# Kernel tuning notes

Measured on AMD Instinct MI355X. Metric: run time of the kernel, lower is better.

## Reference

```python
import jax, jax.numpy as jnp
import numpy as np

N = 50000      # nodes
E = 500000     # edges
IN_FEAT = 128
OUT_FEAT = 128
R = 200        # num_relations
NB = 16        # num_bases -> 8x8 blocks
SI = IN_FEAT // NB   # submat_in = 8
SO = OUT_FEAT // NB  # submat_out = 8


def setup_inputs() -> dict:
    key = jax.random.key(0)
    k1, k2, k3, k4, k5, k6, k7 = jax.random.split(key, 7)
    h = jax.random.normal(k1, (N, IN_FEAT), dtype=jnp.float32)
    norm = jax.random.uniform(k2, (N, 1), dtype=jnp.float32)
    weight = jax.random.normal(k3, (R, NB * SI * SO), dtype=jnp.float32) * 0.1
    loop_weight = jax.random.normal(k4, (IN_FEAT, OUT_FEAT), dtype=jnp.float32) * 0.1
    src = jax.random.randint(k5, (E,), 0, N, dtype=jnp.int32)
    dst = jax.random.randint(k6, (E,), 0, N, dtype=jnp.int32)
    etype = jax.random.randint(k7, (E,), 0, R, dtype=jnp.int32)
    return {"h": h, "norm": norm, "weight": weight, "loop_weight": loop_weight,
            "src": src, "dst": dst, "etype": etype}


def reference(h, norm, weight, loop_weight, src, dst, etype):
    # self-loop message: [N, out_feat]
    loop_message = h @ loop_weight
    # per-edge relation-weight gather: [E, NB, SI, SO]
    w_e = weight[etype].reshape(-1, NB, SI, SO)
    # src features as per-basis blocks: [E, NB, SI]
    x_e = h[src].reshape(-1, NB, SI)
    # block-diagonal bmm -> messages [E, out_feat]
    msg = jnp.einsum('ebi,ebio->ebo', x_e, w_e).reshape(-1, OUT_FEAT)
    # scatter-sum to destination nodes (fn.sum(msg -> h))
    agg = jax.ops.segment_sum(msg, dst, num_segments=N)
    # apply_func: multiply by per-node norm, then add self-loop and activation
    nodes = agg * norm
    nodes = nodes + loop_message
    return jax.nn.relu(nodes)
```

## Files before the change

### kernel.cpp

```cpp
#include <hip/hip_runtime.h>
#include <hip/hip_bf16.h>


#define IN_FEAT 128
#define OUT_FEAT 128
#define SCAN_CHUNK 512

using short8  = __attribute__((ext_vector_type(8))) short;
using float4v = __attribute__((ext_vector_type(4))) float;

__device__ inline float blo(unsigned u) { return __uint_as_float(u << 16); }
__device__ inline float bhi(unsigned u) { return __uint_as_float(u & 0xffff0000u); }
__device__ inline unsigned short f2bf(float f) {
  __hip_bfloat16 b = __float2bfloat16(f);
  return *reinterpret_cast<unsigned short*>(&b);
}

__device__ inline float dot2bf(unsigned x, unsigned w, float c) {
#if __has_builtin(__builtin_amdgcn_fdot2_f32_bf16)
  typedef __bf16 bf16x2 __attribute__((ext_vector_type(2)));
  return __builtin_amdgcn_fdot2_f32_bf16(__builtin_bit_cast(bf16x2, x),
                                         __builtin_bit_cast(bf16x2, w), c, false);
#else
  return c + blo(x) * blo(w) + bhi(x) * bhi(w);
#endif
}

__global__ __launch_bounds__(256) void k_prep(
    const float* __restrict__ w, unsigned short* __restrict__ w16,
    const float* __restrict__ h, uint4* __restrict__ h16p, int htotal8,
    const float* __restrict__ lw, unsigned short* __restrict__ lwT,
    const int* __restrict__ dst, int* __restrict__ cnt, int E,
    int bw, int bh, int blw) {
  __shared__ float srow[1024];
  const int bid = blockIdx.x;
  if (bid < bw) {
    const float* wr = w + ((size_t)bid << 10);
    ((float4*)srow)[threadIdx.x] = ((const float4*)wr)[threadIdx.x];
    __syncthreads();
    const int d0 = threadIdx.x * 4;
    unsigned short o4[4];
    #pragma unroll
    for (int k = 0; k < 4; ++k) {
      const int d = d0 + k;
      const int b = d >> 6;
      const int q = d & 63;
      const int opp = q >> 4;
      const int tt = q & 15;
      const int jj = tt >> 3;
      const int ii = tt & 7;
      o4[k] = f2bf(srow[b * 64 + ii * 8 + opp * 2 + jj]);
    }
    *(uint2*)(w16 + ((size_t)bid << 10) + d0) =
        make_uint2((unsigned)o4[0] | ((unsigned)o4[1] << 16),
                   (unsigned)o4[2] | ((unsigned)o4[3] << 16));
  } else if (bid < bw + bh) {
    const int t = (bid - bw) * 256 + threadIdx.x;
    if (t < htotal8) {
      const float4 a = ((const float4*)h)[2 * t];
      const float4 b = ((const float4*)h)[2 * t + 1];
      uint4 o;
      o.x = (unsigned)f2bf(a.x) | ((unsigned)f2bf(a.y) << 16);
      o.y = (unsigned)f2bf(a.z) | ((unsigned)f2bf(a.w) << 16);
      o.z = (unsigned)f2bf(b.x) | ((unsigned)f2bf(b.y) << 16);
      o.w = (unsigned)f2bf(b.z) | ((unsigned)f2bf(b.w) << 16);
      h16p[t] = o;
    }
  } else if (bid < bw + bh + blw) {
    const int idx = (bid - bw - bh) * 256 + threadIdx.x;
    if (idx < IN_FEAT * OUT_FEAT) {
      const int o = idx >> 7;
      const int k = idx & 127;
      lwT[idx] = f2bf(lw[k * 128 + o]);
    }
  } else {
    const int e0 = ((bid - bw - bh - blw) * 256 + threadIdx.x) * 4;
    if (e0 + 3 < E) {
      const int4 d4 = *(const int4*)(dst + e0);
      atomicAdd(&cnt[d4.x], 1);
      atomicAdd(&cnt[d4.y], 1);
      atomicAdd(&cnt[d4.z], 1);
      atomicAdd(&cnt[d4.w], 1);
    } else {
      for (int e = e0; e < E; ++e) atomicAdd(&cnt[dst[e]], 1);
    }
  }
}

__global__ __launch_bounds__(256) void k_gemm_sum(
    const unsigned short* __restrict__ h16, const unsigned short* __restrict__ lwT,
    float* __restrict__ out, int N,
    const int* __restrict__ cnt, int* __restrict__ bsum, int gemm_blocks) {
  if (blockIdx.x < gemm_blocks) {
    const int wid = threadIdx.x >> 6;
    const int lane = threadIdx.x & 63;
    const int row0 = blockIdx.x * 64 + wid * 16;
    if (row0 >= N) return;
    const int m = lane & 15;
    const int kg = (lane >> 4) * 8;
    const int arow = min(row0 + m, N - 1);

    float4v acc[8];
    #pragma unroll
    for (int nt = 0; nt < 8; ++nt) acc[nt] = (float4v){0.f, 0.f, 0.f, 0.f};

    const unsigned short* ap = h16 + (size_t)arow * 128 + kg;
    const unsigned short* bp = lwT + (size_t)m * 128 + kg;

    #pragma unroll
    for (int kc = 0; kc < 4; ++kc) {
      const short8 a = *(const short8*)(ap + kc * 32);
      #pragma unroll
      for (int nt = 0; nt < 8; ++nt) {
        const short8 b = *(const short8*)(bp + nt * 2048 + kc * 32);
        acc[nt] = __builtin_amdgcn_mfma_f32_16x16x32_bf16(a, b, acc[nt], 0, 0, 0);
      }
    }

    const int crow = row0 + (lane >> 4) * 4;
    #pragma unroll
    for (int nt = 0; nt < 8; ++nt) {
      #pragma unroll
      for (int r = 0; r < 4; ++r) {
        const int row = crow + r;
        if (row < N) out[(size_t)row * 128 + nt * 16 + m] = acc[nt][r];
      }
    }
  } else {
    __shared__ int s[256];
    const int cb = blockIdx.x - gemm_blocks;
    const int t = threadIdx.x;
    const int base = cb * SCAN_CHUNK;
    int v = 0;
    const int i0 = base + t, i1 = base + 256 + t;
    if (i0 < N) v += cnt[i0];
    if (i1 < N) v += cnt[i1];
    s[t] = v;
    __syncthreads();
    for (int d = 128; d > 0; d >>= 1) {
      if (t < d) s[t] += s[t + d];
      __syncthreads();
    }
    if (t == 0) bsum[cb] = s[0];
  }
}

__global__ __launch_bounds__(256) void k_chunksum(
    const int* __restrict__ cnt, int* __restrict__ bsum, int N) {
  __shared__ int s[256];
  const int t = threadIdx.x;
  const int base = blockIdx.x * SCAN_CHUNK;
  int v = 0;
  int i0 = base + t, i1 = base + 256 + t;
  if (i0 < N) v += cnt[i0];
  if (i1 < N) v += cnt[i1];
  s[t] = v;
  __syncthreads();
  for (int d = 128; d > 0; d >>= 1) {
    if (t < d) s[t] += s[t + d];
    __syncthreads();
  }
  if (t == 0) bsum[blockIdx.x] = s[0];
}

__global__ __launch_bounds__(256) void k_hist(
    const int* __restrict__ dst, int* __restrict__ cnt, int E) {
  const int e = blockIdx.x * blockDim.x + threadIdx.x;
  if (e < E) atomicAdd(&cnt[dst[e]], 1);
}

__global__ __launch_bounds__(256) void k_offsets(
    const int* __restrict__ cnt, const int* __restrict__ bsum,
    int* __restrict__ pos, int N) {
  __shared__ int s[256];
  __shared__ int sbase;
  const int t = threadIdx.x;
  if (t < 64) {
    int acc = 0;
    for (int j = t; j < (int)blockIdx.x; j += 64) acc += bsum[j];
    #pragma unroll
    for (int d = 1; d < 64; d <<= 1) acc += __shfl_xor(acc, d);
    if (t == 0) sbase = acc;
  }
  const int base = blockIdx.x * SCAN_CHUNK;
  const int i0 = base + 2 * t;
  const int i1 = i0 + 1;
  const int c0 = (i0 < N) ? cnt[i0] : 0;
  const int c1 = (i1 < N) ? cnt[i1] : 0;
  const int pair = c0 + c1;
  s[t] = pair;
  __syncthreads();
  #pragma unroll
  for (int d = 1; d < 256; d <<= 1) {
    int v = (t >= d) ? s[t - d] : 0;
    __syncthreads();
    s[t] += v;
    __syncthreads();
  }
  const int ex = s[t] - pair + sbase;
  if (i0 < N) pos[i0] = ex;
  if (i1 < N) pos[i1] = ex + c0;
}

__global__ __launch_bounds__(256) void k_scatter(
    const int* __restrict__ src, const int* __restrict__ dst,
    const int* __restrict__ etype, int* __restrict__ pos,
    int2* __restrict__ srcet, int E) {
  const int e0 = (blockIdx.x * blockDim.x + threadIdx.x) * 4;
  if (e0 + 3 < E) {
    const int4 s4 = *(const int4*)(src + e0);
    const int4 d4 = *(const int4*)(dst + e0);
    const int4 t4 = *(const int4*)(etype + e0);
    int p;
    p = atomicAdd(&pos[d4.x], 1); srcet[p] = make_int2(s4.x, t4.x);
    p = atomicAdd(&pos[d4.y], 1); srcet[p] = make_int2(s4.y, t4.y);
    p = atomicAdd(&pos[d4.z], 1); srcet[p] = make_int2(s4.z, t4.z);
    p = atomicAdd(&pos[d4.w], 1); srcet[p] = make_int2(s4.w, t4.w);
  } else {
    for (int e = e0; e < E; ++e) {
      const int p = atomicAdd(&pos[dst[e]], 1);
      srcet[p] = make_int2(src[e], etype[e]);
    }
  }
}

__global__ __launch_bounds__(256) void agg_bf16(
    const unsigned short* __restrict__ h16, const float* __restrict__ norm,
    const unsigned short* __restrict__ w16, const int* __restrict__ pos,
    const int* __restrict__ cnt, const int2* __restrict__ srcet,
    float* __restrict__ out, int N) {
  const int node = (int)((blockIdx.x * blockDim.x + threadIdx.x) >> 6);
  const int lane = threadIdx.x & 63;
  if (node >= N) return;

  const int b = lane >> 2;
  const int opp = lane & 3;
  const int woff = b * 64 + opp * 16;
  const int o = b * 8 + opp * 2;

  const int num = cnt[node];
  const int end = pos[node];
  const int begin = end - num;

  float* outp = out + ((size_t)node << 7) + o;
  const float2 prev = *(const float2*)outp;
  const float nm = norm[node];

  float a0 = 0.f, a1 = 0.f;

  for (int base = 0; base < num; base += 64) {
    const int cn = min(64, num - base);
    const int2 my = srcet[begin + base + min(lane, cn - 1)];
    for (int i4 = 0; i4 < cn; i4 += 4) {
      const int gl = min(i4 + (lane >> 4), cn - 1);
      const int sg = __shfl(my.x, gl);
      const uint4 xq =
          *(const uint4*)(h16 + ((size_t)sg << 7) + (lane & 15) * 8);
      const int nin = min(4, cn - i4);
      #pragma unroll 4
      for (int u = 0; u < nin; ++u) {
        const int r = __shfl(my.y, i4 + u);
        const int sl = u * 16 + b;
        uint4 xv;
        xv.x = __shfl(xq.x, sl);
        xv.y = __shfl(xq.y, sl);
        xv.z = __shfl(xq.z, sl);
        xv.w = __shfl(xq.w, sl);
        const unsigned short* wp = w16 + ((size_t)r << 10) + woff;
        const uint4 wa = *(const uint4*)(wp);
        const uint4 wb = *(const uint4*)(wp + 8);

        a0 = dot2bf(xv.x, wa.x, a0);
        a0 = dot2bf(xv.y, wa.y, a0);
        a0 = dot2bf(xv.z, wa.z, a0);
        a0 = dot2bf(xv.w, wa.w, a0);
        a1 = dot2bf(xv.x, wb.x, a1);
        a1 = dot2bf(xv.y, wb.y, a1);
        a1 = dot2bf(xv.z, wb.z, a1);
        a1 = dot2bf(xv.w, wb.w, a1);
      }
    }
  }

  float2 res;
  res.x = fmaxf(prev.x + a0 * nm, 0.f);
  res.y = fmaxf(prev.y + a1 * nm, 0.f);
  *(float2*)outp = res;
}

__global__ __launch_bounds__(256) void selfloop_gemm(
    const float* __restrict__ h, const float* __restrict__ lw,
    float* __restrict__ out, int n) {
  __shared__ float slw[IN_FEAT * OUT_FEAT];
  __shared__ float sh[32 * IN_FEAT];

  {
    const float4* s4 = (const float4*)lw;
    float4* d4 = (float4*)slw;
    for (int i = threadIdx.x; i < IN_FEAT * OUT_FEAT / 4; i += 256) d4[i] = s4[i];
  }

  const int cg = threadIdx.x & 31;
  const int rg = threadIdx.x >> 5;

  for (int base = blockIdx.x * 32; base < n; base += gridDim.x * 32) {
    const int nrows = min(32, n - base);
    __syncthreads();
    {
      const float4* hs = (const float4*)(h + (size_t)base * IN_FEAT);
      float4* sd = (float4*)sh;
      const int cnt = nrows * (IN_FEAT / 4);
      for (int i = threadIdx.x; i < cnt; i += 256) sd[i] = hs[i];
    }
    __syncthreads();

    float4 acc[4];
    #pragma unroll
    for (int j = 0; j < 4; ++j) acc[j] = make_float4(0.f, 0.f, 0.f, 0.f);

    #pragma unroll 4
    for (int k = 0; k < IN_FEAT; ++k) {
      const float4 w = ((const float4*)slw)[k * 32 + cg];
      #pragma unroll
      for (int j = 0; j < 4; ++j) {
        const float hv = sh[(rg + 8 * j) * IN_FEAT + k];
        acc[j].x += hv * w.x;
        acc[j].y += hv * w.y;
        acc[j].z += hv * w.z;
        acc[j].w += hv * w.w;
      }
    }

    #pragma unroll
    for (int j = 0; j < 4; ++j) {
      const int r = rg + 8 * j;
      if (r < nrows) {
        ((float4*)(out + (size_t)(base + r) * OUT_FEAT))[cg] = acc[j];
      }
    }
  }
}

__global__ __launch_bounds__(256) void agg(
    const float* __restrict__ h, const float* __restrict__ norm,
    const float* __restrict__ weight, const int* __restrict__ pos,
    const int* __restrict__ cnt, const int2* __restrict__ srcet,
    float* __restrict__ out, int N) {
  const int node = (int)((blockIdx.x * blockDim.x + threadIdx.x) >> 6);
  const int lane = threadIdx.x & 63;
  if (node >= N) return;

  const int b = lane >> 2;
  const int op = (lane & 3) * 2;
  const int boff = b * 64 + op;

  const int num = cnt[node];
  const int end = pos[node];
  const int begin = end - num;

  float a0 = 0.f, a1 = 0.f;

  for (int base = 0; base < num; base += 64) {
    const int cn = min(64, num - base);
    const int2 my = srcet[begin + base + min(lane, cn - 1)];
    #pragma unroll 2
    for (int i = 0; i < cn; ++i) {
      const int s = __shfl(my.x, i);
      const int r = __shfl(my.y, i);
      const float* xp = h + ((size_t)s << 7) + b * 8;
      const float4 x0 = ((const float4*)xp)[0];
      const float4 x1 = ((const float4*)xp)[1];
      const float* wp = weight + ((size_t)r << 10) + boff;
      const float2 w0 = *(const float2*)(wp);
      const float2 w1 = *(const float2*)(wp + 8);
      const float2 w2 = *(const float2*)(wp + 16);
      const float2 w3 = *(const float2*)(wp + 24);
      const float2 w4 = *(const float2*)(wp + 32);
      const float2 w5 = *(const float2*)(wp + 40);
      const float2 w6 = *(const float2*)(wp + 48);
      const float2 w7 = *(const float2*)(wp + 56);
      a0 += x0.x * w0.x; a1 += x0.x * w0.y;
      a0 += x0.y * w1.x; a1 += x0.y * w1.y;
      a0 += x0.z * w2.x; a1 += x0.z * w2.y;
      a0 += x0.w * w3.x; a1 += x0.w * w3.y;
      a0 += x1.x * w4.x; a1 += x1.x * w4.y;
      a0 += x1.y * w5.x; a1 += x1.y * w5.y;
      a0 += x1.z * w6.x; a1 += x1.z * w6.y;
      a0 += x1.w * w7.x; a1 += x1.w * w7.y;
    }
  }

  const float nm = norm[node];
  const int o = b * 8 + op;
  float* outp = out + ((size_t)node << 7) + o;
  float2 prev = *(const float2*)outp;
  float2 res;
  res.x = fmaxf(prev.x + a0 * nm, 0.f);
  res.y = fmaxf(prev.y + a1 * nm, 0.f);
  *(float2*)outp = res;
}

__global__ __launch_bounds__(256) void edge_msg(
    const float* __restrict__ h, const float* __restrict__ norm,
    const float* __restrict__ weight, const int* __restrict__ src,
    const int* __restrict__ dst, const int* __restrict__ etype,
    float* out, int E) {
  const int wave = (int)((blockIdx.x * blockDim.x + threadIdx.x) >> 6);
  const int lane = threadIdx.x & 63;
  if (wave >= E) return;

  const int s = src[wave];
  const int d = dst[wave];
  const int r = etype[wave];
  const float nrm = norm[d];

  const int b = lane >> 2;
  const int op = (lane & 3) * 2;

  const float* xp = h + (size_t)s * IN_FEAT + b * 8;
  const float4 x0 = ((const float4*)xp)[0];
  const float4 x1 = ((const float4*)xp)[1];
  float x[8] = {x0.x, x0.y, x0.z, x0.w, x1.x, x1.y, x1.z, x1.w};

  const float* wp = weight + (size_t)r * 1024 + b * 64 + op;
  float a0 = 0.f, a1 = 0.f;
  #pragma unroll
  for (int i = 0; i < 8; ++i) {
    const float2 w = *(const float2*)(wp + i * 8);
    a0 += x[i] * w.x;
    a1 += x[i] * w.y;
  }

  const int o = b * 8 + op;
  float* outp = out + (size_t)d * OUT_FEAT + o;
  atomicAdd(outp, a0 * nrm);
  atomicAdd(outp + 1, a1 * nrm);
}

__global__ __launch_bounds__(256) void relu_k(float* __restrict__ out, int n4) {
  const int i = blockIdx.x * blockDim.x + threadIdx.x;
  if (i < n4) {
    float4 v = ((const float4*)out)[i];
    v.x = fmaxf(v.x, 0.f);
    v.y = fmaxf(v.y, 0.f);
    v.z = fmaxf(v.z, 0.f);
    v.w = fmaxf(v.w, 0.f);
    ((float4*)out)[i] = v;
  }
}

extern "C" void kernel_launch(void* const* d_in, const int* in_sizes, int n_in,
                              void* d_out, int out_size, void* d_ws, size_t ws_size,
                              hipStream_t stream) {
  const float* h    = (const float*)d_in[0];
  const float* norm = (const float*)d_in[1];
  const float* w    = (const float*)d_in[2];
  const float* lw   = (const float*)d_in[3];
  const int* src    = (const int*)d_in[4];
  const int* dst    = (const int*)d_in[5];
  const int* etype  = (const int*)d_in[6];
  float* out = (float*)d_out;

  const int N = in_sizes[1];
  const int E = in_sizes[4];
  const int R = in_sizes[2] / 1024;
  const int nblk = (N + SCAN_CHUNK - 1) / SCAN_CHUNK;

  const size_t nb_bsum = (size_t)((nblk < 128) ? 128 : nblk);
  const size_t off_cnt  = (size_t)E * 8;
  const size_t off_pos  = off_cnt + (size_t)N * 4;
  const size_t off_bsum = off_pos + (size_t)N * 4;
  size_t off_h16 = off_bsum + nb_bsum * 4;
  off_h16 = (off_h16 + 15) & ~(size_t)15;
  const size_t off_w16 = off_h16 + (size_t)N * IN_FEAT * 2;
  const size_t off_lwT = off_w16 + (size_t)R * 1024 * 2;
  const size_t need_full = off_lwT + (size_t)IN_FEAT * OUT_FEAT * 2;
  const size_t need_sort = off_bsum + nb_bsum * 4;

  if (ws_size >= need_full) {
    char* wsb = (char*)d_ws;
    int2* srcet = (int2*)wsb;
    int* cnt  = (int*)(wsb + off_cnt);
    int* pos  = (int*)(wsb + off_pos);
    int* bsum = (int*)(wsb + off_bsum);
    unsigned short* h16 = (unsigned short*)(wsb + off_h16);
    unsigned short* w16 = (unsigned short*)(wsb + off_w16);
    unsigned short* lwT = (unsigned short*)(wsb + off_lwT);

    hipMemsetAsync(cnt, 0, (size_t)N * 4, stream);

    const int htotal8 = N * IN_FEAT / 8;
    const int bw  = R;
    const int bh  = (htotal8 + 255) / 256;
    const int blw = (IN_FEAT * OUT_FEAT + 255) / 256;
    const int bhist = (E + 1023) / 1024;
    k_prep<<<bw + bh + blw + bhist, 256, 0, stream>>>(
        w, w16, h, (uint4*)h16, htotal8, lw, lwT, dst, cnt, E, bw, bh, blw);

    const int gemm_blocks = (N + 63) / 64;
    k_gemm_sum<<<gemm_blocks + nblk, 256, 0, stream>>>(
        h16, lwT, out, N, cnt, bsum, gemm_blocks);

    k_offsets<<<nblk, 256, 0, stream>>>(cnt, bsum, pos, N);
    k_scatter<<<(E + 1023) / 1024, 256, 0, stream>>>(src, dst, etype, pos,
                                                     srcet, E);

    agg_bf16<<<(N + 3) / 4, 256, 0, stream>>>(h16, norm, w16, pos, cnt, srcet,
                                              out, N);
  } else if (ws_size >= need_sort) {
    char* wsb = (char*)d_ws;
    int2* srcet = (int2*)wsb;
    int* cnt  = (int*)(wsb + off_cnt);
    int* pos  = (int*)(wsb + off_pos);
    int* bsum = (int*)(wsb + off_bsum);

    selfloop_gemm<<<512, 256, 0, stream>>>(h, lw, out, N);
    hipMemsetAsync(cnt, 0, (size_t)N * 4, stream);
    k_hist<<<(E + 255) / 256, 256, 0, stream>>>(dst, cnt, E);
    k_chunksum<<<nblk, 256, 0, stream>>>(cnt, bsum, N);
    k_offsets<<<nblk, 256, 0, stream>>>(cnt, bsum, pos, N);
    k_scatter<<<(E + 1023) / 1024, 256, 0, stream>>>(src, dst, etype, pos,
                                                     srcet, E);
    agg<<<(N + 3) / 4, 256, 0, stream>>>(h, norm, w, pos, cnt, srcet, out, N);
  } else {
    selfloop_gemm<<<512, 256, 0, stream>>>(h, lw, out, N);
    edge_msg<<<(E + 3) / 4, 256, 0, stream>>>(h, norm, w, src, dst, etype, out, E);
    const int n4 = N * OUT_FEAT / 4;
    relu_k<<<(n4 + 255) / 256, 256, 0, stream>>>(out, n4);
  }
}
```

Measured before the change: 148.4 us.

## Fuse preprocessing, GEMM, histogram, scan and scatter into one cooperative kernel

Replaces the memset and the four preprocessing launches (bf16 conversion, self-loop MFMA GEMM plus count, offsets, scatter) with a single cooperative persistent kernel that separates phases with grid-wide syncs. The aim is to remove launch gaps and inter-kernel drain overhead. The scan now has each block re-sum all counts before its chunk instead of using a separate chunk-sum pass, which adds redundant reads. The grid is capped at occupancy, so each phase uses grid-stride loops, and the weight conversion is now done element by element. A fallback path keeps the old multi-kernel sequence when cooperative launch is unavailable.

```diff
diff --git a/kernel.cpp b/kernel.cpp
--- a/kernel.cpp
+++ b/kernel.cpp
@@ -1,5 +1,8 @@
 #include <hip/hip_runtime.h>
 #include <hip/hip_bf16.h>
+#include <hip/hip_cooperative_groups.h>
+
+namespace cg = cooperative_groups;
 
 
 #define IN_FEAT 128
@@ -24,6 +27,238 @@
 #else
   return c + blo(x) * blo(w) + bhi(x) * bhi(w);
 #endif
+}
+
+__global__ __launch_bounds__(256, 4) void k_pipeline(
+    const float* __restrict__ w, const float* __restrict__ h,
+    const float* __restrict__ lw, const int* __restrict__ src,
+    const int* __restrict__ dst, const int* __restrict__ etype,
+    unsigned short* __restrict__ w16, uint4* __restrict__ h16p,
+    unsigned short* __restrict__ lwT, int* __restrict__ cnt,
+    int* __restrict__ pos, int2* __restrict__ srcet,
+    float* __restrict__ out, int N, int E, int R) {
+  cg::grid_group grid = cg::this_grid();
+  const int nb = (int)gridDim.x;
+  const int tid = (int)threadIdx.x;
+  const int gtid = (int)blockIdx.x * 256 + tid;
+  const int gstride = nb * 256;
+
+  for (int i = gtid; i < N; i += gstride) cnt[i] = 0;
+
+  const int wtotal = R * 1024;
+  for (int idx = gtid; idx < wtotal; idx += gstride) {
+    const int r = idx >> 10;
+    const int rem = idx & 1023;
+    const int b = rem >> 6;
+    const int q = rem & 63;
+    const int opp = q >> 4;
+    const int t = q & 15;
+    const int j = t >> 3;
+    const int i = t & 7;
+    w16[idx] = f2bf(w[((size_t)r << 10) + b * 64 + i * 8 + opp * 2 + j]);
+  }
+
+  const int htotal8 = N * (IN_FEAT / 8);
+  for (int t8 = gtid; t8 < htotal8; t8 += gstride) {
+    const float4 a = ((const float4*)h)[2 * t8];
+    const float4 b = ((const float4*)h)[2 * t8 + 1];
+    uint4 o;
+    o.x = (unsigned)f2bf(a.x) | ((unsigned)f2bf(a.y) << 16);
+    o.y = (unsigned)f2bf(a.z) | ((unsigned)f2bf(a.w) << 16);
+    o.z = (unsigned)f2bf(b.x) | ((unsigned)f2bf(b.y) << 16);
+    o.w = (unsigned)f2bf(b.z) | ((unsigned)f2bf(b.w) << 16);
+    h16p[t8] = o;
+  }
+
+  for (int idx = gtid; idx < IN_FEAT * OUT_FEAT; idx += gstride) {
+    const int o = idx >> 7;
+    const int k = idx & 127;
+    lwT[idx] = f2bf(lw[k * 128 + o]);
+  }
+
+  grid.sync();
+
+  {
+    const unsigned short* h16 = (const unsigned short*)h16p;
+    const int wid = tid >> 6;
+    const int lane = tid & 63;
+    const int m = lane & 15;
+    const int kg = (lane >> 4) * 8;
+    const int gemm_vb = (N + 63) >> 6;
+    for (int vb = (int)blockIdx.x; vb < gemm_vb; vb += nb) {
+      const int row0 = vb * 64 + wid * 16;
+      if (row0 < N) {
+        const int arow = min(row0 + m, N - 1);
+        float4v acc[8];
+        #pragma unroll
+        for (int nt = 0; nt < 8; ++nt) acc[nt] = (float4v){0.f, 0.f, 0.f, 0.f};
+        const unsigned short* ap = h16 + (size_t)arow * 128 + kg;
+        const unsigned short* bp = lwT + (size_t)m * 128 + kg;
+        #pragma unroll
+        for (int kc = 0; kc < 4; ++kc) {
+          const short8 a = *(const short8*)(ap + kc * 32);
+          #pragma unroll
+          for (int nt = 0; nt < 8; ++nt) {
+            const short8 b = *(const short8*)(bp + nt * 2048 + kc * 32);
+            acc[nt] =
+                __builtin_amdgcn_mfma_f32_16x16x32_bf16(a, b, acc[nt], 0, 0, 0);
+          }
+        }
+        const int crow = row0 + (lane >> 4) * 4;
+        #pragma unroll
+        for (int nt = 0; nt < 8; ++nt) {
+          #pragma unroll
+          for (int r = 0; r < 4; ++r) {
+            const int row = crow + r;
+            if (row < N) out[(size_t)row * 128 + nt * 16 + m] = acc[nt][r];
+          }
+        }
+      }
+    }
+  }
+  {
+    const int e4 = (E + 3) >> 2;
+    for (int g = gtid; g < e4; g += gstride) {
+      const int e0 = g * 4;
+      if (e0 + 3 < E) {
+        const int4 d4 = *(const int4*)(dst + e0);
+        atomicAdd(&cnt[d4.x], 1);
+        atomicAdd(&cnt[d4.y], 1);
+        atomicAdd(&cnt[d4.z], 1);
+        atomicAdd(&cnt[d4.w], 1);
+      } else {
+        for (int e = e0; e < E; ++e) atomicAdd(&cnt[dst[e]], 1);
+      }
+    }
+  }
+
+  grid.sync();
+
+  {
+    __shared__ int s[256];
+    __shared__ int sbase;
+    const int nblk = (N + SCAN_CHUNK - 1) / SCAN_CHUNK;
+    for (int vb = (int)blockIdx.x; vb < nblk; vb += nb) {
+      __syncthreads();
+      const int lim = vb * SCAN_CHUNK;
+      int acc = 0;
+      for (int i = tid; i < lim; i += 256) acc += cnt[i];
+      s[tid] = acc;
+      __syncthreads();
+      for (int d = 128; d > 0; d >>= 1) {
+        if (tid < d) s[tid] += s[tid + d];
+        __syncthreads();
+      }
+      if (tid == 0) sbase = s[0];
+      __syncthreads();
+      const int base = vb * SCAN_CHUNK;
+      const int i0 = base + 2 * tid;
+      const int i1 = i0 + 1;
+      const int c0 = (i0 < N) ? cnt[i0] : 0;
+      const int c1 = (i1 < N) ? cnt[i1] : 0;
+      const int pair = c0 + c1;
+      s[tid] = pair;
+      __syncthreads();
+      #pragma unroll
+      for (int d = 1; d < 256; d <<= 1) {
+        int v = (tid >= d) ? s[tid - d] : 0;
+        __syncthreads();
+        s[tid] += v;
+        __syncthreads();
+      }
+      const int ex = s[tid] - pair + sbase;
+      if (i0 < N) pos[i0] = ex;
+      if (i1 < N) pos[i1] = ex + c0;
+    }
+  }
+
+  grid.sync();
+
+  {
+    const int e4 = (E + 3) >> 2;
+    for (int g = gtid; g < e4; g += gstride) {
+      const int e0 = g * 4;
+      if (e0 + 3 < E) {
+        const int4 s4 = *(const int4*)(src + e0);
+        const int4 d4 = *(const int4*)(dst + e0);
+        const int4 t4 = *(const int4*)(etype + e0);
+        int p;
+        p = atomicAdd(&pos[d4.x], 1); srcet[p] = make_int2(s4.x, t4.x);
+        p = atomicAdd(&pos[d4.y], 1); srcet[p] = make_int2(s4.y, t4.y);
+        p = atomicAdd(&pos[d4.z], 1); srcet[p] = make_int2(s4.z, t4.z);
+        p = atomicAdd(&pos[d4.w], 1); srcet[p] = make_int2(s4.w, t4.w);
+      } else {
+        for (int e = e0; e < E; ++e) {
+          const int p = atomicAdd(&pos[dst[e]], 1);
+          srcet[p] = make_int2(src[e], etype[e]);
+        }
+      }
+    }
+  }
+}
+
+__global__ __launch_bounds__(256) void agg_bf16(
+    const unsigned short* __restrict__ h16, const float* __restrict__ norm,
+    const unsigned short* __restrict__ w16, const int* __restrict__ pos,
+    const int* __restrict__ cnt, const int2* __restrict__ srcet,
+    float* __restrict__ out, int N) {
+  const int node = (int)((blockIdx.x * blockDim.x + threadIdx.x) >> 6);
+  const int lane = threadIdx.x & 63;
+  if (node >= N) return;
+
+  const int b = lane >> 2;
+  const int opp = lane & 3;
+  const int woff = b * 64 + opp * 16;
+  const int o = b * 8 + opp * 2;
+
+  const int num = cnt[node];
+  const int end = pos[node];
+  const int begin = end - num;
+
+  float* outp = out + ((size_t)node << 7) + o;
+  const float2 prev = *(const float2*)outp;
+  const float nm = norm[node];
+
+  float a0 = 0.f, a1 = 0.f;
+
+  for (int base = 0; base < num; base += 64) {
+    const int cn = min(64, num - base);
+    const int2 my = srcet[begin + base + min(lane, cn - 1)];
+    for (int i4 = 0; i4 < cn; i4 += 4) {
+      const int gl = min(i4 + (lane >> 4), cn - 1);
+      const int sg = __shfl(my.x, gl);
+      const uint4 xq =
+          *(const uint4*)(h16 + ((size_t)sg << 7) + (lane & 15) * 8);
+      const int nin = min(4, cn - i4);
+      #pragma unroll 4
+      for (int u = 0; u < nin; ++u) {
+        const int r = __shfl(my.y, i4 + u);
+        const int sl = u * 16 + b;
+        uint4 xv;
+        xv.x = __shfl(xq.x, sl);
+        xv.y = __shfl(xq.y, sl);
+        xv.z = __shfl(xq.z, sl);
+        xv.w = __shfl(xq.w, sl);
+        const unsigned short* wp = w16 + ((size_t)r << 10) + woff;
+        const uint4 wa = *(const uint4*)(wp);
+        const uint4 wb = *(const uint4*)(wp + 8);
+
+        a0 = dot2bf(xv.x, wa.x, a0);
+        a0 = dot2bf(xv.y, wa.y, a0);
+        a0 = dot2bf(xv.z, wa.z, a0);
+        a0 = dot2bf(xv.w, wa.w, a0);
+        a1 = dot2bf(xv.x, wb.x, a1);
+        a1 = dot2bf(xv.y, wb.y, a1);
+        a1 = dot2bf(xv.z, wb.z, a1);
+        a1 = dot2bf(xv.w, wb.w, a1);
+      }
+    }
+  }
+
+  float2 res;
+  res.x = fmaxf(prev.x + a0 * nm, 0.f);
+  res.y = fmaxf(prev.y + a1 * nm, 0.f);
+  *(float2*)outp = res;
 }
 
 __global__ __launch_bounds__(256) void k_prep(
@@ -145,30 +380,6 @@
   }
 }
 
-__global__ __launch_bounds__(256) void k_chunksum(
-    const int* __restrict__ cnt, int* __restrict__ bsum, int N) {
-  __shared__ int s[256];
-  const int t = threadIdx.x;
-  const int base = blockIdx.x * SCAN_CHUNK;
-  int v = 0;
-  int i0 = base + t, i1 = base + 256 + t;
-  if (i0 < N) v += cnt[i0];
-  if (i1 < N) v += cnt[i1];
-  s[t] = v;
-  __syncthreads();
-  for (int d = 128; d > 0; d >>= 1) {
-    if (t < d) s[t] += s[t + d];
-    __syncthreads();
-  }
-  if (t == 0) bsum[blockIdx.x] = s[0];
-}
-
-__global__ __launch_bounds__(256) void k_hist(
-    const int* __restrict__ dst, int* __restrict__ cnt, int E) {
-  const int e = blockIdx.x * blockDim.x + threadIdx.x;
-  if (e < E) atomicAdd(&cnt[dst[e]], 1);
-}
-
 __global__ __launch_bounds__(256) void k_offsets(
     const int* __restrict__ cnt, const int* __restrict__ bsum,
     int* __restrict__ pos, int N) {
@@ -224,68 +435,28 @@
   }
 }
 
-__global__ __launch_bounds__(256) void agg_bf16(
-    const unsigned short* __restrict__ h16, const float* __restrict__ norm,
-    const unsigned short* __restrict__ w16, const int* __restrict__ pos,
-    const int* __restrict__ cnt, const int2* __restrict__ srcet,
-    float* __restrict__ out, int N) {
-  const int node = (int)((blockIdx.x * blockDim.x + threadIdx.x) >> 6);
-  const int lane = threadIdx.x & 63;
-  if (node >= N) return;
-
-  const int b = lane >> 2;
-  const int opp = lane & 3;
-  const int woff = b * 64 + opp * 16;
-  const int o = b * 8 + opp * 2;
-
-  const int num = cnt[node];
-  const int end = pos[node];
-  const int begin = end - num;
-
-  float* outp = out + ((size_t)node << 7) + o;
-  const float2 prev = *(const float2*)outp;
-  const float nm = norm[node];
-
-  float a0 = 0.f, a1 = 0.f;
-
-  for (int base = 0; base < num; base += 64) {
-    const int cn = min(64, num - base);
-    const int2 my = srcet[begin + base + min(lane, cn - 1)];
-    for (int i4 = 0; i4 < cn; i4 += 4) {
-      const int gl = min(i4 + (lane >> 4), cn - 1);
-      const int sg = __shfl(my.x, gl);
-      const uint4 xq =
-          *(const uint4*)(h16 + ((size_t)sg << 7) + (lane & 15) * 8);
-      const int nin = min(4, cn - i4);
-      #pragma unroll 4
-      for (int u = 0; u < nin; ++u) {
-        const int r = __shfl(my.y, i4 + u);
-        const int sl = u * 16 + b;
-        uint4 xv;
-        xv.x = __shfl(xq.x, sl);
-        xv.y = __shfl(xq.y, sl);
-        xv.z = __shfl(xq.z, sl);
-        xv.w = __shfl(xq.w, sl);
-        const unsigned short* wp = w16 + ((size_t)r << 10) + woff;
-        const uint4 wa = *(const uint4*)(wp);
-        const uint4 wb = *(const uint4*)(wp + 8);
-
-        a0 = dot2bf(xv.x, wa.x, a0);
-        a0 = dot2bf(xv.y, wa.y, a0);
-        a0 = dot2bf(xv.z, wa.z, a0);
-        a0 = dot2bf(xv.w, wa.w, a0);
-        a1 = dot2bf(xv.x, wb.x, a1);
-        a1 = dot2bf(xv.y, wb.y, a1);
-        a1 = dot2bf(xv.z, wb.z, a1);
-        a1 = dot2bf(xv.w, wb.w, a1);
-      }
-    }
-  }
-
-  float2 res;
-  res.x = fmaxf(prev.x + a0 * nm, 0.f);
-  res.y = fmaxf(prev.y + a1 * nm, 0.f);
-  *(float2*)outp = res;
+__global__ __launch_bounds__(256) void k_hist(
+    const int* __restrict__ dst, int* __restrict__ cnt, int E) {
+  const int e = blockIdx.x * blockDim.x + threadIdx.x;
+  if (e < E) atomicAdd(&cnt[dst[e]], 1);
+}
+
+__global__ __launch_bounds__(256) void k_chunksum(
+    const int* __restrict__ cnt, int* __restrict__ bsum, int N) {
+  __shared__ int s[256];
+  const int t = threadIdx.x;
+  const int base = blockIdx.x * SCAN_CHUNK;
+  int v = 0;
+  int i0 = base + t, i1 = base + 256 + t;
+  if (i0 < N) v += cnt[i0];
+  if (i1 < N) v += cnt[i1];
+  s[t] = v;
+  __syncthreads();
+  for (int d = 128; d > 0; d >>= 1) {
+    if (t < d) s[t] += s[t + d];
+    __syncthreads();
+  }
+  if (t == 0) bsum[blockIdx.x] = s[0];
 }
 
 __global__ __launch_bounds__(256) void selfloop_gemm(
@@ -300,7 +471,7 @@
     for (int i = threadIdx.x; i < IN_FEAT * OUT_FEAT / 4; i += 256) d4[i] = s4[i];
   }
 
-  const int cg = threadIdx.x & 31;
+  const int cg_ = threadIdx.x & 31;
   const int rg = threadIdx.x >> 5;
 
   for (int base = blockIdx.x * 32; base < n; base += gridDim.x * 32) {
@@ -320,7 +491,7 @@
 
     #pragma unroll 4
     for (int k = 0; k < IN_FEAT; ++k) {
-      const float4 w = ((const float4*)slw)[k * 32 + cg];
+      const float4 w = ((const float4*)slw)[k * 32 + cg_];
       #pragma unroll
       for (int j = 0; j < 4; ++j) {
         const float hv = sh[(rg + 8 * j) * IN_FEAT + k];
@@ -335,7 +506,7 @@
     for (int j = 0; j < 4; ++j) {
       const int r = rg + 8 * j;
       if (r < nrows) {
-        ((float4*)(out + (size_t)(base + r) * OUT_FEAT))[cg] = acc[j];
+        ((float4*)(out + (size_t)(base + r) * OUT_FEAT))[cg_] = acc[j];
       }
     }
   }
@@ -487,26 +658,45 @@
     unsigned short* w16 = (unsigned short*)(wsb + off_w16);
     unsigned short* lwT = (unsigned short*)(wsb + off_lwT);
 
-    hipMemsetAsync(cnt, 0, (size_t)N * 4, stream);
-
-    const int htotal8 = N * IN_FEAT / 8;
-    const int bw  = R;
-    const int bh  = (htotal8 + 255) / 256;
-    const int blw = (IN_FEAT * OUT_FEAT + 255) / 256;
-    const int bhist = (E + 1023) / 1024;
-    k_prep<<<bw + bh + blw + bhist, 256, 0, stream>>>(
-        w, w16, h, (uint4*)h16, htotal8, lw, lwT, dst, cnt, E, bw, bh, blw);
-
-    const int gemm_blocks = (N + 63) / 64;
-    k_gemm_sum<<<gemm_blocks + nblk, 256, 0, stream>>>(
-        h16, lwT, out, N, cnt, bsum, gemm_blocks);
-
-    k_offsets<<<nblk, 256, 0, stream>>>(cnt, bsum, pos, N);
-    k_scatter<<<(E + 1023) / 1024, 256, 0, stream>>>(src, dst, etype, pos,
-                                                     srcet, E);
-
-    agg_bf16<<<(N + 3) / 4, 256, 0, stream>>>(h16, norm, w16, pos, cnt, srcet,
-                                              out, N);
+    int dev = 0;
+    hipGetDevice(&dev);
+    int coop = 0;
+    hipDeviceGetAttribute(&coop, hipDeviceAttributeCooperativeLaunch, dev);
+    int ncu = 0, maxb = 0;
+    if (coop) {
+      hipDeviceGetAttribute(&ncu, hipDeviceAttributeMultiprocessorCount, dev);
+      hipOccupancyMaxActiveBlocksPerMultiprocessor(&maxb, k_pipeline, 256, 0);
+    }
+    const int grid = ncu * maxb;
+
+    if (coop && grid > 0) {
+      uint4* h16p = (uint4*)h16;
+      void* args[] = {(void*)&w,   (void*)&h,    (void*)&lw,  (void*)&src,
+                      (void*)&dst, (void*)&etype,(void*)&w16, (void*)&h16p,
+                      (void*)&lwT, (void*)&cnt,  (void*)&pos, (void*)&srcet,
+                      (void*)&out, (void*)&N,    (void*)&E,   (void*)&R};
+      hipLaunchCooperativeKernel((void*)k_pipeline, dim3(grid), dim3(256),
+                                 args, 0, stream);
+      agg_bf16<<<(N + 3) / 4, 256, 0, stream>>>(h16, norm, w16, pos, cnt,
+                                                srcet, out, N);
+    } else {
+      hipMemsetAsync(cnt, 0, (size_t)N * 4, stream);
+      const int htotal8 = N * IN_FEAT / 8;
+      const int bw  = R;
+      const int bh  = (htotal8 + 255) / 256;
+      const int blw = (IN_FEAT * OUT_FEAT + 255) / 256;
+      const int bhist = (E + 1023) / 1024;
+      k_prep<<<bw + bh + blw + bhist, 256, 0, stream>>>(
+          w, w16, h, (uint4*)h16, htotal8, lw, lwT, dst, cnt, E, bw, bh, blw);
+      const int gemm_blocks = (N + 63) / 64;
+      k_gemm_sum<<<gemm_blocks + nblk, 256, 0, stream>>>(
+          h16, lwT, out, N, cnt, bsum, gemm_blocks);
+      k_offsets<<<nblk, 256, 0, stream>>>(cnt, bsum, pos, N);
+      k_scatter<<<(E + 1023) / 1024, 256, 0, stream>>>(src, dst, etype, pos,
+                                                       srcet, E);
+      agg_bf16<<<(N + 3) / 4, 256, 0, stream>>>(h16, norm, w16, pos, cnt,
+                                                srcet, out, N);
+    }
   } else if (ws_size >= need_sort) {
     char* wsb = (char*)d_ws;
     int2* srcet = (int2*)wsb;
```

New measurement: 328.6 us. +121.5%, slower.

## Fuse self-loop GEMM into aggregation kernel and drop separate chunk-sum pass

Applied to the files above, without the earlier changes.

Moves the self-loop h@loop_weight MFMA GEMM into the aggregation kernel. Each 256-thread block computes a 16-row tile into shared memory and then aggregates those 16 nodes, so the loop message is never written to and re-read from global memory. It also replaces the chunk-sum plus offsets pair with one offsets kernel, where each block recomputes its prefix by reading all earlier counts. That saves a launch and the global round trip, but the prefix work grows quadratically with block count, and each wave now handles 4 nodes serially, which may reduce latency hiding in the gather loop.

```diff
diff --git a/kernel.cpp b/kernel.cpp
--- a/kernel.cpp
+++ b/kernel.cpp
@@ -87,102 +87,26 @@
   }
 }
 
-__global__ __launch_bounds__(256) void k_gemm_sum(
-    const unsigned short* __restrict__ h16, const unsigned short* __restrict__ lwT,
-    float* __restrict__ out, int N,
-    const int* __restrict__ cnt, int* __restrict__ bsum, int gemm_blocks) {
-  if (blockIdx.x < gemm_blocks) {
-    const int wid = threadIdx.x >> 6;
-    const int lane = threadIdx.x & 63;
-    const int row0 = blockIdx.x * 64 + wid * 16;
-    if (row0 >= N) return;
-    const int m = lane & 15;
-    const int kg = (lane >> 4) * 8;
-    const int arow = min(row0 + m, N - 1);
-
-    float4v acc[8];
-    #pragma unroll
-    for (int nt = 0; nt < 8; ++nt) acc[nt] = (float4v){0.f, 0.f, 0.f, 0.f};
-
-    const unsigned short* ap = h16 + (size_t)arow * 128 + kg;
-    const unsigned short* bp = lwT + (size_t)m * 128 + kg;
-
-    #pragma unroll
-    for (int kc = 0; kc < 4; ++kc) {
-      const short8 a = *(const short8*)(ap + kc * 32);
-      #pragma unroll
-      for (int nt = 0; nt < 8; ++nt) {
-        const short8 b = *(const short8*)(bp + nt * 2048 + kc * 32);
-        acc[nt] = __builtin_amdgcn_mfma_f32_16x16x32_bf16(a, b, acc[nt], 0, 0, 0);
-      }
-    }
-
-    const int crow = row0 + (lane >> 4) * 4;
-    #pragma unroll
-    for (int nt = 0; nt < 8; ++nt) {
-      #pragma unroll
-      for (int r = 0; r < 4; ++r) {
-        const int row = crow + r;
-        if (row < N) out[(size_t)row * 128 + nt * 16 + m] = acc[nt][r];
-      }
-    }
-  } else {
-    __shared__ int s[256];
-    const int cb = blockIdx.x - gemm_blocks;
-    const int t = threadIdx.x;
-    const int base = cb * SCAN_CHUNK;
-    int v = 0;
-    const int i0 = base + t, i1 = base + 256 + t;
-    if (i0 < N) v += cnt[i0];
-    if (i1 < N) v += cnt[i1];
-    s[t] = v;
+__global__ __launch_bounds__(256) void k_offsets_sp(
+    const int* __restrict__ cnt, int* __restrict__ pos, int N) {
+  __shared__ int s[256];
+  __shared__ int sbase;
+  const int t = threadIdx.x;
+  const int vb = blockIdx.x;
+  {
+    const int lim = vb * SCAN_CHUNK;
+    int acc = 0;
+    for (int i = t; i < lim; i += 256) acc += cnt[i];
+    s[t] = acc;
     __syncthreads();
     for (int d = 128; d > 0; d >>= 1) {
       if (t < d) s[t] += s[t + d];
       __syncthreads();
     }
-    if (t == 0) bsum[cb] = s[0];
-  }
-}
-
-__global__ __launch_bounds__(256) void k_chunksum(
-    const int* __restrict__ cnt, int* __restrict__ bsum, int N) {
-  __shared__ int s[256];
-  const int t = threadIdx.x;
-  const int base = blockIdx.x * SCAN_CHUNK;
-  int v = 0;
-  int i0 = base + t, i1 = base + 256 + t;
-  if (i0 < N) v += cnt[i0];
-  if (i1 < N) v += cnt[i1];
-  s[t] = v;
-  __syncthreads();
-  for (int d = 128; d > 0; d >>= 1) {
-    if (t < d) s[t] += s[t + d];
-    __syncthreads();
-  }
-  if (t == 0) bsum[blockIdx.x] = s[0];
-}
-
-__global__ __launch_bounds__(256) void k_hist(
-    const int* __restrict__ dst, int* __restrict__ cnt, int E) {
-  const int e = blockIdx.x * blockDim.x + threadIdx.x;
-  if (e < E) atomicAdd(&cnt[dst[e]], 1);
-}
-
-__global__ __launch_bounds__(256) void k_offsets(
-    const int* __restrict__ cnt, const int* __restrict__ bsum,
-    int* __restrict__ pos, int N) {
-  __shared__ int s[256];
-  __shared__ int sbase;
-  const int t = threadIdx.x;
-  if (t < 64) {
-    int acc = 0;
-    for (int j = t; j < (int)blockIdx.x; j += 64) acc += bsum[j];
-    #pragma unroll
-    for (int d = 1; d < 64; d <<= 1) acc += __shfl_xor(acc, d);
-    if (t == 0) sbase = acc;
-  }
-  const int base = blockIdx.x * SCAN_CHUNK;
+    if (t == 0) sbase = s[0];
+    __syncthreads();
+  }
+  const int base = vb * SCAN_CHUNK;
   const int i0 = base + 2 * t;
   const int i1 = i0 + 1;
   const int c0 = (i0 < N) ? cnt[i0] : 0;
@@ -224,68 +148,105 @@
   }
 }
 
-__global__ __launch_bounds__(256) void agg_bf16(
+__global__ __launch_bounds__(256) void agg_fused(
     const unsigned short* __restrict__ h16, const float* __restrict__ norm,
-    const unsigned short* __restrict__ w16, const int* __restrict__ pos,
-    const int* __restrict__ cnt, const int2* __restrict__ srcet,
-    float* __restrict__ out, int N) {
-  const int node = (int)((blockIdx.x * blockDim.x + threadIdx.x) >> 6);
+    const unsigned short* __restrict__ w16, const unsigned short* __restrict__ lwT,
+    const int* __restrict__ pos, const int* __restrict__ cnt,
+    const int2* __restrict__ srcet, float* __restrict__ out, int N) {
+  __shared__ float lmsg[16][128];
+  const int wid = threadIdx.x >> 6;
   const int lane = threadIdx.x & 63;
-  if (node >= N) return;
+  const int node_base = blockIdx.x * 16;
+
+  {
+    const int m = lane & 15;
+    const int kg = (lane >> 4) * 8;
+    const int arow = min(node_base + m, N - 1);
+    const unsigned short* ap = h16 + (size_t)arow * 128 + kg;
+    const unsigned short* bp = lwT + (size_t)m * 128 + kg;
+    const int nt0 = wid * 2, nt1 = wid * 2 + 1;
+
+    float4v acc0 = (float4v){0.f, 0.f, 0.f, 0.f};
+    float4v acc1 = (float4v){0.f, 0.f, 0.f, 0.f};
+    #pragma unroll
+    for (int kc = 0; kc < 4; ++kc) {
+      const short8 a  = *(const short8*)(ap + kc * 32);
+      const short8 b0 = *(const short8*)(bp + nt0 * 2048 + kc * 32);
+      const short8 b1 = *(const short8*)(bp + nt1 * 2048 + kc * 32);
+      acc0 = __builtin_amdgcn_mfma_f32_16x16x32_bf16(a, b0, acc0, 0, 0, 0);
+      acc1 = __builtin_amdgcn_mfma_f32_16x16x32_bf16(a, b1, acc1, 0, 0, 0);
+    }
+    const int rrow = (lane >> 4) * 4;
+    #pragma unroll
+    for (int r = 0; r < 4; ++r) {
+      lmsg[rrow + r][nt0 * 16 + m] = acc0[r];
+      lmsg[rrow + r][nt1 * 16 + m] = acc1[r];
+    }
+  }
+  __syncthreads();
 
   const int b = lane >> 2;
   const int opp = lane & 3;
   const int woff = b * 64 + opp * 16;
   const int o = b * 8 + opp * 2;
 
-  const int num = cnt[node];
-  const int end = pos[node];
-  const int begin = end - num;
-
-  float* outp = out + ((size_t)node << 7) + o;
-  const float2 prev = *(const float2*)outp;
-  const float nm = norm[node];
-
-  float a0 = 0.f, a1 = 0.f;
-
-  for (int base = 0; base < num; base += 64) {
-    const int cn = min(64, num - base);
-    const int2 my = srcet[begin + base + min(lane, cn - 1)];
-    for (int i4 = 0; i4 < cn; i4 += 4) {
-      const int gl = min(i4 + (lane >> 4), cn - 1);
-      const int sg = __shfl(my.x, gl);
-      const uint4 xq =
-          *(const uint4*)(h16 + ((size_t)sg << 7) + (lane & 15) * 8);
-      const int nin = min(4, cn - i4);
-      #pragma unroll 4
-      for (int u = 0; u < nin; ++u) {
-        const int r = __shfl(my.y, i4 + u);
-        const int sl = u * 16 + b;
-        uint4 xv;
-        xv.x = __shfl(xq.x, sl);
-        xv.y = __shfl(xq.y, sl);
-        xv.z = __shfl(xq.z, sl);
-        xv.w = __shfl(xq.w, sl);
-        const unsigned short* wp = w16 + ((size_t)r << 10) + woff;
-        const uint4 wa = *(const uint4*)(wp);
-        const uint4 wb = *(const uint4*)(wp + 8);
-
-        a0 = dot2bf(xv.x, wa.x, a0);
-        a0 = dot2bf(xv.y, wa.y, a0);
-        a0 = dot2bf(xv.z, wa.z, a0);
-        a0 = dot2bf(xv.w, wa.w, a0);
-        a1 = dot2bf(xv.x, wb.x, a1);
-        a1 = dot2bf(xv.y, wb.y, a1);
-        a1 = dot2bf(xv.z, wb.z, a1);
-        a1 = dot2bf(xv.w, wb.w, a1);
+  for (int u = 0; u < 4; ++u) {
+    const int node = node_base + wid * 4 + u;
+    if (node >= N) continue;
+
+    const int num = cnt[node];
+    const int end = pos[node];
+    const int begin = end - num;
+
+    float a0 = 0.f, a1 = 0.f;
+
+    for (int base = 0; base < num; base += 64) {
+      const int cn = min(64, num - base);
+      const int2 my = srcet[begin + base + min(lane, cn - 1)];
+      for (int i4 = 0; i4 < cn; i4 += 4) {
+        const int gl = min(i4 + (lane >> 4), cn - 1);
+        const int sg = __shfl(my.x, gl);
+        const uint4 xq =
+            *(const uint4*)(h16 + ((size_t)sg << 7) + (lane & 15) * 8);
+        const int nin = min(4, cn - i4);
+        #pragma unroll 4
+        for (int v = 0; v < nin; ++v) {
+          const int r = __shfl(my.y, i4 + v);
+          const int sl = v * 16 + b;
+          uint4 xv;
+          xv.x = __shfl(xq.x, sl);
+          xv.y = __shfl(xq.y, sl);
+          xv.z = __shfl(xq.z, sl);
+          xv.w = __shfl(xq.w, sl);
+          const unsigned short* wp = w16 + ((size_t)r << 10) + woff;
+          const uint4 wa = *(const uint4*)(wp);
+          const uint4 wb = *(const uint4*)(wp + 8);
+
+          a0 = dot2bf(xv.x, wa.x, a0);
+          a0 = dot2bf(xv.y, wa.y, a0);
+          a0 = dot2bf(xv.z, wa.z, a0);
+          a0 = dot2bf(xv.w, wa.w, a0);
+          a1 = dot2bf(xv.x, wb.x, a1);
+          a1 = dot2bf(xv.y, wb.y, a1);
+          a1 = dot2bf(xv.z, wb.z, a1);
+          a1 = dot2bf(xv.w, wb.w, a1);
+        }
       }
     }
-  }
-
-  float2 res;
-  res.x = fmaxf(prev.x + a0 * nm, 0.f);
-  res.y = fmaxf(prev.y + a1 * nm, 0.f);
-  *(float2*)outp = res;
+
+    const float nm = norm[node];
+    const float2 prev = *(const float2*)&lmsg[wid * 4 + u][o];
+    float2 res;
+    res.x = fmaxf(prev.x + a0 * nm, 0.f);
+    res.y = fmaxf(prev.y + a1 * nm, 0.f);
+    *(float2*)(out + ((size_t)node << 7) + o) = res;
+  }
+}
+
+__global__ __launch_bounds__(256) void k_hist(
+    const int* __restrict__ dst, int* __restrict__ cnt, int E) {
+  const int e = blockIdx.x * blockDim.x + threadIdx.x;
+  if (e < E) atomicAdd(&cnt[dst[e]], 1);
 }
 
 __global__ __launch_bounds__(256) void selfloop_gemm(
@@ -300,7 +261,7 @@
     for (int i = threadIdx.x; i < IN_FEAT * OUT_FEAT / 4; i += 256) d4[i] = s4[i];
   }
 
-  const int cg = threadIdx.x & 31;
+  const int cg_ = threadIdx.x & 31;
   const int rg = threadIdx.x >> 5;
 
   for (int base = blockIdx.x * 32; base < n; base += gridDim.x * 32) {
@@ -320,7 +281,7 @@
 
     #pragma unroll 4
     for (int k = 0; k < IN_FEAT; ++k) {
-      const float4 w = ((const float4*)slw)[k * 32 + cg];
+      const float4 w = ((const float4*)slw)[k * 32 + cg_];
       #pragma unroll
       for (int j = 0; j < 4; ++j) {
         const float hv = sh[(rg + 8 * j) * IN_FEAT + k];
@@ -335,7 +296,7 @@
     for (int j = 0; j < 4; ++j) {
       const int r = rg + 8 * j;
       if (r < nrows) {
-        ((float4*)(out + (size_t)(base + r) * OUT_FEAT))[cg] = acc[j];
+        ((float4*)(out + (size_t)(base + r) * OUT_FEAT))[cg_] = acc[j];
       }
     }
   }
@@ -482,7 +443,6 @@
     int2* srcet = (int2*)wsb;
     int* cnt  = (int*)(wsb + off_cnt);
     int* pos  = (int*)(wsb + off_pos);
-    int* bsum = (int*)(wsb + off_bsum);
     unsigned short* h16 = (unsigned short*)(wsb + off_h16);
     unsigned short* w16 = (unsigned short*)(wsb + off_w16);
     unsigned short* lwT = (unsigned short*)(wsb + off_lwT);
@@ -497,28 +457,22 @@
     k_prep<<<bw + bh + blw + bhist, 256, 0, stream>>>(
         w, w16, h, (uint4*)h16, htotal8, lw, lwT, dst, cnt, E, bw, bh, blw);
 
-    const int gemm_blocks = (N + 63) / 64;
-    k_gemm_sum<<<gemm_blocks + nblk, 256, 0, stream>>>(
-        h16, lwT, out, N, cnt, bsum, gemm_blocks);
-
-    k_offsets<<<nblk, 256, 0, stream>>>(cnt, bsum, pos, N);
+    k_offsets_sp<<<nblk, 256, 0, stream>>>(cnt, pos, N);
     k_scatter<<<(E + 1023) / 1024, 256, 0, stream>>>(src, dst, etype, pos,
                                                      srcet, E);
 
-    agg_bf16<<<(N + 3) / 4, 256, 0, stream>>>(h16, norm, w16, pos, cnt, srcet,
-                                              out, N);
+    agg_fused<<<(N + 15) / 16, 256, 0, stream>>>(h16, norm, w16, lwT, pos, cnt,
+                                                 srcet, out, N);
   } else if (ws_size >= need_sort) {
     char* wsb = (char*)d_ws;
     int2* srcet = (int2*)wsb;
     int* cnt  = (int*)(wsb + off_cnt);
     int* pos  = (int*)(wsb + off_pos);
-    int* bsum = (int*)(wsb + off_bsum);
 
     selfloop_gemm<<<512, 256, 0, stream>>>(h, lw, out, N);
     hipMemsetAsync(cnt, 0, (size_t)N * 4, stream);
     k_hist<<<(E + 255) / 256, 256, 0, stream>>>(dst, cnt, E);
-    k_chunksum<<<nblk, 256, 0, stream>>>(cnt, bsum, N);
-    k_offsets<<<nblk, 256, 0, stream>>>(cnt, bsum, pos, N);
+    k_offsets_sp<<<nblk, 256, 0, stream>>>(cnt, pos, N);
     k_scatter<<<(E + 1023) / 1024, 256, 0, stream>>>(src, dst, etype, pos,
                                                      srcet, E);
     agg<<<(N + 3) / 4, 256, 0, stream>>>(h, norm, w, pos, cnt, srcet, out, N);
```

Result: slower. 169.9 us (+14.5%).
